# Kernel tuning notes

Hardware: AMD Instinct MI355X
Metric: run time of the kernel (lower is better)

The kernel has to match this reference:

```python
import jax, jax.numpy as jnp
import numpy as np

B, C_IN, C_OUT, H, W = 4, 256, 256, 56, 56
NH, K, P = 2, 5, 2
HD = C_OUT // NH          # 128
SE_H = C_OUT // 16        # 16
SE_H2 = max(SE_H // 16, 1)  # 1
EPS = 1e-5


def setup_inputs() -> dict:
    key = jax.random.key(0)
    ks = jax.random.split(key, 16)
    n = lambda k, sh, s=1.0: jax.random.normal(k, sh, jnp.float32) * s

    def bn_params(k, c):
        k1, k2 = jax.random.split(k)
        return (1.0 + 0.1 * n(k1, (c,)), 0.1 * n(k2, (c,)),
                jnp.zeros((c,), jnp.float32), jnp.ones((c,), jnp.float32))

    agg_g1, agg_b1, agg_m1, agg_v1 = bn_params(ks[6], C_OUT)
    agg_g2, agg_b2, agg_m2, agg_v2 = bn_params(ks[7], C_OUT)
    se_g_in, se_b_in, se_m_in, se_v_in = bn_params(ks[8], SE_H)
    se_g_out, se_b_out, se_m_out, se_v_out = bn_params(ks[9], C_OUT)
    return {
        "x": n(ks[0], (B, C_IN, H, W)),
        "Wq": n(ks[1], (C_OUT, C_IN), C_IN ** -0.5),
        "Wk": n(ks[2], (C_OUT, C_IN), C_IN ** -0.5),
        "Wv": n(ks[3], (C_OUT, C_IN), C_IN ** -0.5),
        "rel_h": n(ks[4], (HD, 1, 1, K, 1)),
        "rel_w": n(ks[5], (HD, 1, 1, 1, K)),
        "agg_g1": agg_g1, "agg_b1": agg_b1, "agg_m1": agg_m1, "agg_v1": agg_v1,
        "agg_W": n(ks[10], (C_OUT, C_OUT), C_OUT ** -0.5),
        "agg_g2": agg_g2, "agg_b2": agg_b2, "agg_m2": agg_m2, "agg_v2": agg_v2,
        "se_Win": n(ks[11], (SE_H, C_OUT), C_OUT ** -0.5),
        "se_g_in": se_g_in, "se_b_in": se_b_in, "se_m_in": se_m_in, "se_v_in": se_v_in,
        "se_fc1": n(ks[12], (SE_H2, SE_H), SE_H ** -0.5),
        "se_fc2": n(ks[13], (SE_H, SE_H2)),
        "se_Wout": n(ks[14], (C_OUT, SE_H), SE_H ** -0.5),
        "se_g_out": se_g_out, "se_b_out": se_b_out, "se_m_out": se_m_out, "se_v_out": se_v_out,
    }


def _conv1x1(Wm, t):
    return jnp.einsum('oc,bchw->bohw', Wm, t)


def _bn(t, g, b, m, v):
    # eval-mode BatchNorm2d with running stats
    return (t - m[:, None, None]) * (g * jax.lax.rsqrt(v + EPS))[:, None, None] + b[:, None, None]


def _windows(t):
    # (B, O, H+2P, W+2P) -> (B, O, H, W, K, K), matching torch unfold(2,K,1).unfold(3,K,1)
    w = jnp.stack([t[:, :, i:i + H, j:j + W] for i in range(K) for j in range(K)], axis=-1)
    return w.reshape(t.shape[0], t.shape[1], H, W, K, K)


def reference(x, Wq, Wk, Wv, rel_h, rel_w,
              agg_g1, agg_b1, agg_m1, agg_v1, agg_W, agg_g2, agg_b2, agg_m2, agg_v2,
              se_Win, se_g_in, se_b_in, se_m_in, se_v_in, se_fc1, se_fc2, se_Wout,
              se_g_out, se_b_out, se_m_out, se_v_out):
    xp = jnp.pad(x, ((0, 0), (0, 0), (P, P), (P, P)))
    q = _conv1x1(Wq, x).reshape(B, NH, HD, H, W)          # (B,NH,HD,H,W)
    k_win = _windows(_conv1x1(Wk, xp))                    # (B,O,H,W,K,K)
    v_win = _windows(_conv1x1(Wv, xp))
    # relative position bias: first head gets rel_h (height taps), second gets rel_w
    k_win = jnp.concatenate([k_win[:, :HD] + rel_h[None], k_win[:, HD:] + rel_w[None]], axis=1)
    k_r = k_win.reshape(B, NH, HD, H, W, K * K)
    v_r = v_win.reshape(B, NH, HD, H, W, K * K)
    scores = jnp.einsum('bnchw,bnchwk->bnhwk', q, k_r) / jnp.sqrt(jnp.float32(HD))
    attn = jax.nn.softmax(scores, axis=-1)
    out = jnp.einsum('bnhwk,bnchwk->bnchw', attn, v_r).reshape(B, C_OUT, H, W)
    # agg: BN -> ReLU -> 1x1 conv -> BN
    y = jax.nn.relu(_bn(out, agg_g1, agg_b1, agg_m1, agg_v1))
    y = _bn(_conv1x1(agg_W, y), agg_g2, agg_b2, agg_m2, agg_v2)
    # squeeze-excitation (intended math; original view(b,c) is a channel-count bug)
    s = jax.nn.relu(_bn(_conv1x1(se_Win, y), se_g_in, se_b_in, se_m_in, se_v_in))  # (B,SE_H,H,W)
    p = s.mean(axis=(2, 3))                                                        # (B,SE_H)
    g = jax.nn.sigmoid(jax.nn.relu(p @ se_fc1.T) @ se_fc2.T)                       # (B,SE_H)
    s = s * g[:, :, None, None]
    return _bn(_conv1x1(se_Wout, s), se_g_out, se_b_out, se_m_out, se_v_out)
```

## Files before the change

### kernel.cpp

```cpp
#include <hip/hip_runtime.h>
#include <hip/hip_bf16.h>

#define HW 3136
#define HH 56
#define WW 56
#define BB 4
#define CC 256
#define HD 128

#define TH 4
#define TW 8
#define WR 8
#define WC 12
#define WPX 96
#define KSTR2 136
#define RSTR 132

#define ASTR 72

typedef __attribute__((ext_vector_type(8))) short bf16x8;
typedef __attribute__((ext_vector_type(4))) float f32x4;

__device__ __forceinline__ unsigned short f2bf(float f) {
    unsigned int u; __builtin_memcpy(&u, &f, 4);
    unsigned int r = u + 0x7FFFu + ((u >> 16) & 1u);
    return (unsigned short)(r >> 16);
}
__device__ __forceinline__ float bflo(unsigned int u) {
    unsigned int x = u << 16; float f; __builtin_memcpy(&f, &x, 4); return f;
}
__device__ __forceinline__ float bfhi(unsigned int u) {
    unsigned int x = u & 0xFFFF0000u; float f; __builtin_memcpy(&f, &x, 4); return f;
}

__global__ __launch_bounds__(256) void xt_cvt(const float* __restrict__ x,
                                              unsigned short* __restrict__ xt)
{
    int b = blockIdx.z;
    int c0 = blockIdx.y * 64;
    int p0 = blockIdx.x * 64;
    __shared__ float tile[64][65];
    int t = threadIdx.x;
    int p4 = t & 15, cl = t >> 4;
    const float* xb = x + ((size_t)b * CC + c0) * HW + p0;
#pragma unroll
    for (int i = 0; i < 4; i++) {
        int c = cl + 16 * i;
        float4 f = *(const float4*)(xb + (size_t)c * HW + p4 * 4);
        tile[c][p4 * 4 + 0] = f.x; tile[c][p4 * 4 + 1] = f.y;
        tile[c][p4 * 4 + 2] = f.z; tile[c][p4 * 4 + 3] = f.w;
    }
    __syncthreads();
    int c2 = t & 31, pl = t >> 5;
    unsigned short* xo = xt + ((size_t)b * HW + p0) * CC + c0;
#pragma unroll
    for (int i = 0; i < 8; i++) {
        int p = pl + 8 * i;
        float a = tile[2 * c2][p], bb = tile[2 * c2 + 1][p];
        unsigned int pk = (unsigned int)f2bf(a) | ((unsigned int)f2bf(bb) << 16);
        *(unsigned int*)(xo + (size_t)p * CC + 2 * c2) = pk;
    }
}

__global__ __launch_bounds__(256) void wcvt(const float* __restrict__ Wq,
                                            const float* __restrict__ Wk,
                                            const float* __restrict__ Wv,
                                            const float* __restrict__ Wa,
                                            const float* __restrict__ Wse,
                                            unsigned short* __restrict__ wb,
                                            float* __restrict__ psum)
{
    int t = threadIdx.x;
    if (blockIdx.y == 4) {
        if (blockIdx.x == 0 && t < 64) psum[t] = 0.f;
        int idx = blockIdx.x * 256 + t;
        if (idx < 1024) {
            float4 f = *(const float4*)(Wse + (size_t)idx * 4);
            uint2 pk;
            pk.x = (unsigned int)f2bf(f.x) | ((unsigned int)f2bf(f.y) << 16);
            pk.y = (unsigned int)f2bf(f.z) | ((unsigned int)f2bf(f.w) << 16);
            *(uint2*)(wb + (size_t)4 * 65536 + (size_t)idx * 4) = pk;
        }
        return;
    }
    const float* srcs[4] = {Wq, Wk, Wv, Wa};
    const float* s = srcs[blockIdx.y];
    int idx = blockIdx.x * 256 + t;
    float4 f = *(const float4*)(s + (size_t)idx * 4);
    uint2 pk;
    pk.x = (unsigned int)f2bf(f.x) | ((unsigned int)f2bf(f.y) << 16);
    pk.y = (unsigned int)f2bf(f.z) | ((unsigned int)f2bf(f.w) << 16);
    *(uint2*)(wb + (size_t)blockIdx.y * 65536 + (size_t)idx * 4) = pk;
}

__global__ __launch_bounds__(256) void qkv_mfma(
    const unsigned short* __restrict__ xt, const unsigned short* __restrict__ wqkv,
    unsigned short* __restrict__ q_ws, unsigned short* __restrict__ k_ws,
    unsigned short* __restrict__ v_ws)
{
    int wsel = blockIdx.z;
    unsigned short* outp = (wsel == 0) ? q_ws : ((wsel == 1) ? k_ws : v_ws);
    int gp0 = blockIdx.x * 128, o0 = blockIdx.y * 128;

    __shared__ unsigned short As[128 * ASTR];
    __shared__ unsigned short Bs[128 * ASTR];
    const unsigned short* xb = xt + (size_t)gp0 * CC;
    const unsigned short* wbp = wqkv + (size_t)wsel * 65536 + (size_t)o0 * CC;

    int t = threadIdx.x;
    int wave = t >> 6, lane = t & 63;
    int mo = (wave & 1) * 64, no = (wave >> 1) * 64;
    int lm = lane & 15, lq = lane >> 4;
    int sr = t >> 3, sc = t & 7;

    f32x4 acc[4][4];
#pragma unroll
    for (int i = 0; i < 4; i++)
#pragma unroll
        for (int j = 0; j < 4; j++) acc[i][j] = (f32x4){0.f, 0.f, 0.f, 0.f};

    for (int k0 = 0; k0 < 256; k0 += 64) {
#pragma unroll
        for (int i = 0; i < 4; i++) {
            int r = sr + 32 * i;
            *(uint4*)&As[r * ASTR + sc * 8] = *(const uint4*)(xb + (size_t)r * CC + k0 + sc * 8);
            *(uint4*)&Bs[r * ASTR + sc * 8] = *(const uint4*)(wbp + (size_t)r * CC + k0 + sc * 8);
        }
        __syncthreads();
#pragma unroll
        for (int ks = 0; ks < 64; ks += 32) {
            bf16x8 af[4], bfr[4];
#pragma unroll
            for (int i = 0; i < 4; i++)
                af[i] = *(bf16x8*)&As[(mo + 16 * i + lm) * ASTR + ks + lq * 8];
#pragma unroll
            for (int j = 0; j < 4; j++)
                bfr[j] = *(bf16x8*)&Bs[(no + 16 * j + lm) * ASTR + ks + lq * 8];
#pragma unroll
            for (int i = 0; i < 4; i++)
#pragma unroll
                for (int j = 0; j < 4; j++)
                    acc[i][j] = __builtin_amdgcn_mfma_f32_16x16x32_bf16(
                        af[i], bfr[j], acc[i][j], 0, 0, 0);
        }
        __syncthreads();
    }
    unsigned short* ob = outp + (size_t)gp0 * CC + o0;
    bool ev = (lm & 1) == 0;
    int elm = lm & ~1;
#pragma unroll
    for (int i = 0; i < 4; i++)
#pragma unroll
        for (int j = 0; j < 4; j++)
#pragma unroll
            for (int r = 0; r < 4; r++) {
                float v = acc[i][j][r];
                float p = __shfl_xor(v, 1, 64);
                unsigned int pk = ev
                    ? ((unsigned int)f2bf(v) | ((unsigned int)f2bf(p) << 16))
                    : ((unsigned int)f2bf(p) | ((unsigned int)f2bf(v) << 16));
                if (ev == (r < 2)) {
                    int m = mo + 16 * i + lq * 4 + r;
                    int n = no + 16 * j + elm;
                    *(unsigned int*)(ob + (size_t)m * CC + n) = pk;
                }
            }
}

__global__ __launch_bounds__(256) void agg_mfma(
    const unsigned short* __restrict__ ao, const unsigned short* __restrict__ wagg,
    const float* __restrict__ g1, const float* __restrict__ b1,
    const float* __restrict__ m1, const float* __restrict__ v1,
    const float* __restrict__ g2, const float* __restrict__ b2,
    const float* __restrict__ m2, const float* __restrict__ v2,
    float* __restrict__ y2)
{
    int gp0 = blockIdx.x * 128, o0 = blockIdx.y * 128;

    __shared__ unsigned short As[128 * ASTR];
    __shared__ unsigned short Bs[128 * ASTR];
    __shared__ float s1[256], o1[256], s2[256], o2[256];

    int t = threadIdx.x;
    {
        float sc1 = g1[t] * rsqrtf(v1[t] + 1e-5f);
        s1[t] = sc1; o1[t] = b1[t] - m1[t] * sc1;
        float sc2 = g2[t] * rsqrtf(v2[t] + 1e-5f);
        s2[t] = sc2; o2[t] = b2[t] - m2[t] * sc2;
    }

    const unsigned short* aob = ao + (size_t)gp0 * CC;
    const unsigned short* wbp = wagg + (size_t)o0 * CC;

    int wave = t >> 6, lane = t & 63;
    int mo = (wave & 1) * 64, no = (wave >> 1) * 64;
    int lm = lane & 15, lq = lane >> 4;
    int sr = t >> 3, sc = t & 7;

    f32x4 acc[4][4];
#pragma unroll
    for (int i = 0; i < 4; i++)
#pragma unroll
        for (int j = 0; j < 4; j++) acc[i][j] = (f32x4){0.f, 0.f, 0.f, 0.f};

    __syncthreads();

    for (int k0 = 0; k0 < 256; k0 += 64) {
#pragma unroll
        for (int i = 0; i < 4; i++) {
            int r = sr + 32 * i;
            int cb = k0 + sc * 8;
            uint4 u = *(const uint4*)(aob + (size_t)r * CC + cb);
            float e[8] = {bflo(u.x), bfhi(u.x), bflo(u.y), bfhi(u.y),
                          bflo(u.z), bfhi(u.z), bflo(u.w), bfhi(u.w)};
            unsigned short pk[8];
#pragma unroll
            for (int uu = 0; uu < 8; uu++) {
                float vv = fmaxf(e[uu] * s1[cb + uu] + o1[cb + uu], 0.f);
                pk[uu] = f2bf(vv);
            }
            *(uint4*)&As[r * ASTR + sc * 8] = *(uint4*)pk;
            *(uint4*)&Bs[r * ASTR + sc * 8] = *(const uint4*)(wbp + (size_t)r * CC + k0 + sc * 8);
        }
        __syncthreads();
#pragma unroll
        for (int ks = 0; ks < 64; ks += 32) {
            bf16x8 af[4], bfr[4];
#pragma unroll
            for (int i = 0; i < 4; i++)
                af[i] = *(bf16x8*)&As[(mo + 16 * i + lm) * ASTR + ks + lq * 8];
#pragma unroll
            for (int j = 0; j < 4; j++)
                bfr[j] = *(bf16x8*)&Bs[(no + 16 * j + lm) * ASTR + ks + lq * 8];
#pragma unroll
            for (int i = 0; i < 4; i++)
#pragma unroll
                for (int j = 0; j < 4; j++)
                    acc[i][j] = __builtin_amdgcn_mfma_f32_16x16x32_bf16(
                        af[i], bfr[j], acc[i][j], 0, 0, 0);
        }
        __syncthreads();
    }
    float* yb = y2 + (size_t)gp0 * CC + o0;
#pragma unroll
    for (int i = 0; i < 4; i++)
#pragma unroll
        for (int j = 0; j < 4; j++)
#pragma unroll
            for (int r = 0; r < 4; r++) {
                int m = mo + 16 * i + lq * 4 + r;
                int n = no + 16 * j + lm;
                yb[(size_t)m * CC + n] = acc[i][j][r] * s2[o0 + n] + o2[o0 + n];
            }
}

__global__ __launch_bounds__(256) void attn_kernel(
    const unsigned short* __restrict__ q_ws, const unsigned short* __restrict__ k_ws,
    const unsigned short* __restrict__ v_ws,
    const float* __restrict__ rel_h, const float* __restrict__ rel_w,
    unsigned short* __restrict__ ao_ws)
{
    __shared__ unsigned short kwin[WPX * KSTR2];
    __shared__ float relT[5 * RSTR];

    int t = threadIdx.x;
    int tile = blockIdx.x;
    int n = blockIdx.y;
    int b = blockIdx.z;
    int tr = tile / 7, tc = tile - tr * 7;
    int h0 = tr * TH, w0 = tc * TW;
    const float* rel = (n == 0) ? rel_h : rel_w;
    const size_t base = (size_t)b * HW * CC + n * HD;

    {
        int c8 = t & 15, pw0 = t >> 4;
#pragma unroll
        for (int it = 0; it < 6; it++) {
            int pw = pw0 + it * 16;
            int wr = pw / 12, wc = pw - wr * 12;
            int gh = h0 + wr - 2, gw = w0 + wc - 2;
            uint4 u = make_uint4(0u, 0u, 0u, 0u);
            if (gh >= 0 && gh < HH && gw >= 0 && gw < WW)
                u = *(const uint4*)(k_ws + base + (size_t)(gh * WW + gw) * CC + c8 * 8);
            *(uint4*)&kwin[pw * KSTR2 + c8 * 8] = u;
        }
        if (t < 128) {
#pragma unroll
            for (int tt = 0; tt < 5; tt++)
                relT[tt * RSTR + t] = rel[t * 5 + tt];
        }
    }
    __syncthreads();

    int px = t >> 3, c4g = t & 7;
    int pr = px >> 3, pc = px & 7;
    int ghp = h0 + pr, gwp = w0 + pc;
    const size_t pbase = base + (size_t)(ghp * WW + gwp) * CC;

    float4 q4[4];
#pragma unroll
    for (int i = 0; i < 4; i++) {
        uint2 uq = *(const uint2*)(q_ws + pbase + (c4g + 8 * i) * 4);
        q4[i] = make_float4(bflo(uq.x), bfhi(uq.x), bflo(uq.y), bfhi(uq.y));
    }

    float acc[30];
#pragma unroll
    for (int tt = 0; tt < 30; tt++) acc[tt] = 0.f;
#pragma unroll
    for (int i = 0; i < 4; i++) {
        float4 q = q4[i];
        int co = (c4g + 8 * i) * 4;
#pragma unroll
        for (int tt = 0; tt < 25; tt++) {
            int di = tt / 5, dj = tt - 5 * (tt / 5);
            int wpx = (pr + di) * WC + pc + dj;
            uint2 ku = *(const uint2*)&kwin[wpx * KSTR2 + co];
            acc[tt] += q.x * bflo(ku.x) + q.y * bfhi(ku.x)
                     + q.z * bflo(ku.y) + q.w * bfhi(ku.y);
        }
#pragma unroll
        for (int tt = 0; tt < 5; tt++) {
            float4 r4 = *(const float4*)&relT[tt * RSTR + co];
            acc[25 + tt] += q.x * r4.x + q.y * r4.y + q.z * r4.z + q.w * r4.w;
        }
    }
#pragma unroll
    for (int tt = 0; tt < 30; tt++) {
#pragma unroll
        for (int m = 1; m < 8; m <<= 1)
            acc[tt] += __shfl_xor(acc[tt], m, 64);
    }
    {
        const float inv = 0.08838834764831845f;
        float mx = -1e30f;
#pragma unroll
        for (int tt = 0; tt < 25; tt++) {
            int di = tt / 5, dj = tt - 5 * (tt / 5);
            acc[tt] = (acc[tt] + ((n == 0) ? acc[25 + di] : acc[25 + dj])) * inv;
            mx = fmaxf(mx, acc[tt]);
        }
        float sum = 0.f;
#pragma unroll
        for (int tt = 0; tt < 25; tt++) { acc[tt] = __expf(acc[tt] - mx); sum += acc[tt]; }
        float rs = 1.f / sum;
#pragma unroll
        for (int tt = 0; tt < 25; tt++) acc[tt] *= rs;
    }
    __syncthreads();

    {
        int c8 = t & 15, pw0 = t >> 4;
#pragma unroll
        for (int it = 0; it < 6; it++) {
            int pw = pw0 + it * 16;
            int wr = pw / 12, wc = pw - wr * 12;
            int gh = h0 + wr - 2, gw = w0 + wc - 2;
            uint4 u = make_uint4(0u, 0u, 0u, 0u);
            if (gh >= 0 && gh < HH && gw >= 0 && gw < WW)
                u = *(const uint4*)(v_ws + base + (size_t)(gh * WW + gw) * CC + c8 * 8);
            *(uint4*)&kwin[pw * KSTR2 + c8 * 8] = u;
        }
    }
    __syncthreads();

    float4 oacc[4];
#pragma unroll
    for (int i = 0; i < 4; i++) oacc[i] = make_float4(0.f, 0.f, 0.f, 0.f);
#pragma unroll
    for (int tt = 0; tt < 25; tt++) {
        int di = tt / 5, dj = tt - 5 * (tt / 5);
        int wpx = (pr + di) * WC + pc + dj;
        float a = acc[tt];
#pragma unroll
        for (int i = 0; i < 4; i++) {
            uint2 vu = *(const uint2*)&kwin[wpx * KSTR2 + (c4g + 8 * i) * 4];
            oacc[i].x += a * bflo(vu.x); oacc[i].y += a * bfhi(vu.x);
            oacc[i].z += a * bflo(vu.y); oacc[i].w += a * bfhi(vu.y);
        }
    }
#pragma unroll
    for (int i = 0; i < 4; i++) {
        uint2 pk;
        pk.x = (unsigned int)f2bf(oacc[i].x) | ((unsigned int)f2bf(oacc[i].y) << 16);
        pk.y = (unsigned int)f2bf(oacc[i].z) | ((unsigned int)f2bf(oacc[i].w) << 16);
        *(uint2*)(ao_ws + pbase + (c4g + 8 * i) * 4) = pk;
    }
}

__global__ __launch_bounds__(256) void se_in_mfma(
    const float* __restrict__ y2, const unsigned short* __restrict__ wse,
    const float* __restrict__ gin, const float* __restrict__ bin,
    const float* __restrict__ min_, const float* __restrict__ vin,
    float* __restrict__ s_ws, float* __restrict__ psum)
{
    int wave = threadIdx.x >> 6, lane = threadIdx.x & 63;
    int tile = blockIdx.x * 4 + wave;
    int gp0 = tile * 16;
    int b = tile / 196;
    int lm = lane & 15, lq = lane >> 4;

    f32x4 acc = (f32x4){0.f, 0.f, 0.f, 0.f};
    const float* ya = y2 + (size_t)(gp0 + lm) * CC;
#pragma unroll
    for (int k0 = 0; k0 < 256; k0 += 32) {
        int kb = k0 + lq * 8;
        float4 f0 = *(const float4*)(ya + kb);
        float4 f1 = *(const float4*)(ya + kb + 4);
        unsigned short pk[8] = {f2bf(f0.x), f2bf(f0.y), f2bf(f0.z), f2bf(f0.w),
                                f2bf(f1.x), f2bf(f1.y), f2bf(f1.z), f2bf(f1.w)};
        bf16x8 af = *(bf16x8*)pk;
        bf16x8 bf = *(const bf16x8*)(wse + (size_t)lm * CC + kb);
        acc = __builtin_amdgcn_mfma_f32_16x16x32_bf16(af, bf, acc, 0, 0, 0);
    }
    float sc = gin[lm] * rsqrtf(vin[lm] + 1e-5f);
    float off = bin[lm] - min_[lm] * sc;
    float sum4 = 0.f;
#pragma unroll
    for (int r = 0; r < 4; r++) {
        int row = lq * 4 + r;
        float v = fmaxf(acc[r] * sc + off, 0.f);
        s_ws[(size_t)(gp0 + row) * 16 + lm] = v;
        sum4 += v;
    }
    sum4 += __shfl_xor(sum4, 16, 64);
    sum4 += __shfl_xor(sum4, 32, 64);
    if (lane < 16) atomicAdd(&psum[b * 16 + lane], sum4);
}

__global__ __launch_bounds__(256) void se_out_kernel(
    const float* __restrict__ s_ws, const float* __restrict__ psum,
    const float* __restrict__ fc1, const float* __restrict__ fc2,
    const float* __restrict__ se_Wout,
    const float* __restrict__ gout, const float* __restrict__ bout,
    const float* __restrict__ mout, const float* __restrict__ vout,
    float* __restrict__ out)
{
    int b = blockIdx.y;
    int px0 = blockIdx.x * 32;
    __shared__ float sl[32 * 17];
    __shared__ float wg[256 * 20];
    __shared__ float bo[256];
    __shared__ float gg[16];
    int t = threadIdx.x;

    if (t < 16) {
        float h = 0.f;
#pragma unroll
        for (int jj = 0; jj < 16; jj++)
            h += (psum[b * 16 + jj] * (1.f / 3136.f)) * fc1[jj];
        h = fmaxf(h, 0.f);
        float z = h * fc2[t];
        gg[t] = 1.f / (1.f + __expf(-z));
    }
    {
        const float* sb = s_ws + (size_t)(b * HW + px0) * 16;
#pragma unroll
        for (int i = 0; i < 2; i++) {
            int idx = t + 256 * i;
            sl[(idx >> 4) * 17 + (idx & 15)] = sb[idx];
        }
    }
    __syncthreads();
    {
        float sc = gout[t] * rsqrtf(vout[t] + 1e-5f);
        bo[t] = bout[t] - mout[t] * sc;
        const float* wr = se_Wout + (size_t)t * 16;
#pragma unroll
        for (int k = 0; k < 16; k++)
            wg[t * 20 + k] = wr[k] * gg[k] * sc;
    }
    __syncthreads();

    int px = t & 31, og = t >> 5;
    float4 s0 = *(float4*)&sl[px * 17 + 0];
    float4 s1v = *(float4*)&sl[px * 17 + 4];
    float4 s2v = *(float4*)&sl[px * 17 + 8];
    float4 s3 = *(float4*)&sl[px * 17 + 12];
    float* ob = out + (size_t)b * CC * HW + px0 + px;
#pragma unroll
    for (int oi = 0; oi < 32; oi++) {
        int o = og * 32 + oi;
        float4 w0 = *(float4*)&wg[o * 20 + 0];
        float4 w1 = *(float4*)&wg[o * 20 + 4];
        float4 w2 = *(float4*)&wg[o * 20 + 8];
        float4 w3 = *(float4*)&wg[o * 20 + 12];
        float r = bo[o]
            + s0.x * w0.x + s0.y * w0.y + s0.z * w0.z + s0.w * w0.w
            + s1v.x * w1.x + s1v.y * w1.y + s1v.z * w1.z + s1v.w * w1.w
            + s2v.x * w2.x + s2v.y * w2.y + s2v.z * w2.z + s2v.w * w2.w
            + s3.x * w3.x + s3.y * w3.y + s3.z * w3.z + s3.w * w3.w;
        ob[(size_t)o * HW] = r;
    }
}

extern "C" void kernel_launch(void* const* d_in, const int* in_sizes, int n_in,
                              void* d_out, int out_size, void* d_ws, size_t ws_size,
                              hipStream_t stream) {
    const float* x     = (const float*)d_in[0];
    const float* Wq    = (const float*)d_in[1];
    const float* Wk    = (const float*)d_in[2];
    const float* Wv    = (const float*)d_in[3];
    const float* rel_h = (const float*)d_in[4];
    const float* rel_w = (const float*)d_in[5];
    const float* agg_g1 = (const float*)d_in[6];
    const float* agg_b1 = (const float*)d_in[7];
    const float* agg_m1 = (const float*)d_in[8];
    const float* agg_v1 = (const float*)d_in[9];
    const float* agg_W  = (const float*)d_in[10];
    const float* agg_g2 = (const float*)d_in[11];
    const float* agg_b2 = (const float*)d_in[12];
    const float* agg_m2 = (const float*)d_in[13];
    const float* agg_v2 = (const float*)d_in[14];
    const float* se_Win = (const float*)d_in[15];
    const float* se_g_in = (const float*)d_in[16];
    const float* se_b_in = (const float*)d_in[17];
    const float* se_m_in = (const float*)d_in[18];
    const float* se_v_in = (const float*)d_in[19];
    const float* se_fc1  = (const float*)d_in[20];
    const float* se_fc2  = (const float*)d_in[21];
    const float* se_Wout = (const float*)d_in[22];
    const float* se_g_out = (const float*)d_in[23];
    const float* se_b_out = (const float*)d_in[24];
    const float* se_m_out = (const float*)d_in[25];
    const float* se_v_out = (const float*)d_in[26];

    const size_t NQ = (size_t)BB * HW * CC;
    unsigned short* q_ws  = (unsigned short*)d_ws;
    unsigned short* k_ws  = q_ws + NQ;
    unsigned short* v_ws  = k_ws + NQ;
    unsigned short* ao_ws = v_ws + NQ;
    unsigned short* xt    = ao_ws;
    float* y2_ws = (float*)d_ws;
    float* s_ws  = (float*)(ao_ws + NQ);
    float* psum  = s_ws + (size_t)BB * HW * 16;
    unsigned short* wbf = (unsigned short*)(psum + 64);

    xt_cvt<<<dim3(49, 4, 4), 256, 0, stream>>>(x, xt);
    wcvt<<<dim3(64, 5), 256, 0, stream>>>(Wq, Wk, Wv, agg_W, se_Win, wbf, psum);
    qkv_mfma<<<dim3(98, 2, 3), 256, 0, stream>>>(xt, wbf, q_ws, k_ws, v_ws);
    attn_kernel<<<dim3(98, 2, 4), 256, 0, stream>>>(q_ws, k_ws, v_ws, rel_h, rel_w, ao_ws);
    agg_mfma<<<dim3(98, 2), 256, 0, stream>>>(ao_ws, wbf + 3 * 65536,
        agg_g1, agg_b1, agg_m1, agg_v1, agg_g2, agg_b2, agg_m2, agg_v2, y2_ws);
    se_in_mfma<<<dim3(196), 256, 0, stream>>>(y2_ws, wbf + 4 * 65536,
        se_g_in, se_b_in, se_m_in, se_v_in, s_ws, psum);
    se_out_kernel<<<dim3(98, 4), 256, 0, stream>>>(s_ws, psum, se_fc1, se_fc2,
        se_Wout, se_g_out, se_b_out, se_m_out, se_v_out, (float*)d_out);
}
```

Baseline: 211.1 us.

## Halve attention tile height and give each thread 8 contiguous channels

The attention kernel tile shrinks from 4x8 to 2x8 pixels, and the grid doubles to 196 tiles per image. Each pixel now gets 16 threads, each owning 8 contiguous channels, instead of 8 threads with four strided 4-channel slices. This allows 128-bit LDS and global loads and more blocks for latency hiding. The cost is extra halo loading per output pixel (a 6x12 window for 16 pixels) and one more shuffle-reduction stage per score.

Measured after the change: 199.6 us. 1.06x faster.

```diff
diff --git a/kernel.cpp b/kernel.cpp
--- a/kernel.cpp
+++ b/kernel.cpp
@@ -8,11 +8,11 @@
 #define CC 256
 #define HD 128
 
-#define TH 4
+#define TH 2
 #define TW 8
-#define WR 8
+#define WR 6
 #define WC 12
-#define WPX 96
+#define WPX 72
 #define KSTR2 136
 #define RSTR 132
 
@@ -273,16 +273,18 @@
     const size_t base = (size_t)b * HW * CC + n * HD;
 
     {
-        int c8 = t & 15, pw0 = t >> 4;
-#pragma unroll
-        for (int it = 0; it < 6; it++) {
-            int pw = pw0 + it * 16;
-            int wr = pw / 12, wc = pw - wr * 12;
-            int gh = h0 + wr - 2, gw = w0 + wc - 2;
-            uint4 u = make_uint4(0u, 0u, 0u, 0u);
-            if (gh >= 0 && gh < HH && gw >= 0 && gw < WW)
-                u = *(const uint4*)(k_ws + base + (size_t)(gh * WW + gw) * CC + c8 * 8);
-            *(uint4*)&kwin[pw * KSTR2 + c8 * 8] = u;
+        int c16 = t & 15, pwt = t >> 4;
+#pragma unroll
+        for (int it = 0; it < 5; it++) {
+            int pw = pwt + it * 16;
+            if (pw < WPX) {
+                int wr = pw / 12, wc = pw - wr * 12;
+                int gh = h0 + wr - 2, gw = w0 + wc - 2;
+                uint4 u = make_uint4(0u, 0u, 0u, 0u);
+                if (gh >= 0 && gh < HH && gw >= 0 && gw < WW)
+                    u = *(const uint4*)(k_ws + base + (size_t)(gh * WW + gw) * CC + c16 * 8);
+                *(uint4*)&kwin[pw * KSTR2 + c16 * 8] = u;
+            }
         }
         if (t < 128) {
 #pragma unroll
@@ -292,43 +294,40 @@
     }
     __syncthreads();
 
-    int px = t >> 3, c4g = t & 7;
+    int px = t >> 4, cg = t & 15;
     int pr = px >> 3, pc = px & 7;
     int ghp = h0 + pr, gwp = w0 + pc;
     const size_t pbase = base + (size_t)(ghp * WW + gwp) * CC;
 
-    float4 q4[4];
-#pragma unroll
-    for (int i = 0; i < 4; i++) {
-        uint2 uq = *(const uint2*)(q_ws + pbase + (c4g + 8 * i) * 4);
-        q4[i] = make_float4(bflo(uq.x), bfhi(uq.x), bflo(uq.y), bfhi(uq.y));
+    float q[8];
+    {
+        uint4 uq = *(const uint4*)(q_ws + pbase + cg * 8);
+        q[0] = bflo(uq.x); q[1] = bfhi(uq.x); q[2] = bflo(uq.y); q[3] = bfhi(uq.y);
+        q[4] = bflo(uq.z); q[5] = bfhi(uq.z); q[6] = bflo(uq.w); q[7] = bfhi(uq.w);
     }
 
     float acc[30];
 #pragma unroll
-    for (int tt = 0; tt < 30; tt++) acc[tt] = 0.f;
-#pragma unroll
-    for (int i = 0; i < 4; i++) {
-        float4 q = q4[i];
-        int co = (c4g + 8 * i) * 4;
-#pragma unroll
-        for (int tt = 0; tt < 25; tt++) {
-            int di = tt / 5, dj = tt - 5 * (tt / 5);
-            int wpx = (pr + di) * WC + pc + dj;
-            uint2 ku = *(const uint2*)&kwin[wpx * KSTR2 + co];
-            acc[tt] += q.x * bflo(ku.x) + q.y * bfhi(ku.x)
-                     + q.z * bflo(ku.y) + q.w * bfhi(ku.y);
-        }
-#pragma unroll
-        for (int tt = 0; tt < 5; tt++) {
-            float4 r4 = *(const float4*)&relT[tt * RSTR + co];
-            acc[25 + tt] += q.x * r4.x + q.y * r4.y + q.z * r4.z + q.w * r4.w;
-        }
+    for (int tt = 0; tt < 25; tt++) {
+        int di = tt / 5, dj = tt - 5 * (tt / 5);
+        int wpx = (pr + di) * WC + pc + dj;
+        uint4 ku = *(const uint4*)&kwin[wpx * KSTR2 + cg * 8];
+        acc[tt] = q[0] * bflo(ku.x) + q[1] * bfhi(ku.x)
+                + q[2] * bflo(ku.y) + q[3] * bfhi(ku.y)
+                + q[4] * bflo(ku.z) + q[5] * bfhi(ku.z)
+                + q[6] * bflo(ku.w) + q[7] * bfhi(ku.w);
+    }
+#pragma unroll
+    for (int tt = 0; tt < 5; tt++) {
+        float4 r0 = *(const float4*)&relT[tt * RSTR + cg * 8];
+        float4 r1 = *(const float4*)&relT[tt * RSTR + cg * 8 + 4];
+        acc[25 + tt] = q[0] * r0.x + q[1] * r0.y + q[2] * r0.z + q[3] * r0.w
+                     + q[4] * r1.x + q[5] * r1.y + q[6] * r1.z + q[7] * r1.w;
     }
 #pragma unroll
     for (int tt = 0; tt < 30; tt++) {
 #pragma unroll
-        for (int m = 1; m < 8; m <<= 1)
+        for (int m = 1; m < 16; m <<= 1)
             acc[tt] += __shfl_xor(acc[tt], m, 64);
     }
     {
@@ -350,42 +349,42 @@
     __syncthreads();
 
     {
-        int c8 = t & 15, pw0 = t >> 4;
-#pragma unroll
-        for (int it = 0; it < 6; it++) {
-            int pw = pw0 + it * 16;
-            int wr = pw / 12, wc = pw - wr * 12;
-            int gh = h0 + wr - 2, gw = w0 + wc - 2;
-            uint4 u = make_uint4(0u, 0u, 0u, 0u);
-            if (gh >= 0 && gh < HH && gw >= 0 && gw < WW)
-                u = *(const uint4*)(v_ws + base + (size_t)(gh * WW + gw) * CC + c8 * 8);
-            *(uint4*)&kwin[pw * KSTR2 + c8 * 8] = u;
-        }
-    }
-    __syncthreads();
-
-    float4 oacc[4];
-#pragma unroll
-    for (int i = 0; i < 4; i++) oacc[i] = make_float4(0.f, 0.f, 0.f, 0.f);
+        int c16 = t & 15, pwt = t >> 4;
+#pragma unroll
+        for (int it = 0; it < 5; it++) {
+            int pw = pwt + it * 16;
+            if (pw < WPX) {
+                int wr = pw / 12, wc = pw - wr * 12;
+                int gh = h0 + wr - 2, gw = w0 + wc - 2;
+                uint4 u = make_uint4(0u, 0u, 0u, 0u);
+                if (gh >= 0 && gh < HH && gw >= 0 && gw < WW)
+                    u = *(const uint4*)(v_ws + base + (size_t)(gh * WW + gw) * CC + c16 * 8);
+                *(uint4*)&kwin[pw * KSTR2 + c16 * 8] = u;
+            }
+        }
+    }
+    __syncthreads();
+
+    float o[8];
+#pragma unroll
+    for (int i = 0; i < 8; i++) o[i] = 0.f;
 #pragma unroll
     for (int tt = 0; tt < 25; tt++) {
         int di = tt / 5, dj = tt - 5 * (tt / 5);
         int wpx = (pr + di) * WC + pc + dj;
         float a = acc[tt];
-#pragma unroll
-        for (int i = 0; i < 4; i++) {
-            uint2 vu = *(const uint2*)&kwin[wpx * KSTR2 + (c4g + 8 * i) * 4];
-            oacc[i].x += a * bflo(vu.x); oacc[i].y += a * bfhi(vu.x);
-            oacc[i].z += a * bflo(vu.y); oacc[i].w += a * bfhi(vu.y);
-        }
-    }
-#pragma unroll
-    for (int i = 0; i < 4; i++) {
-        uint2 pk;
-        pk.x = (unsigned int)f2bf(oacc[i].x) | ((unsigned int)f2bf(oacc[i].y) << 16);
-        pk.y = (unsigned int)f2bf(oacc[i].z) | ((unsigned int)f2bf(oacc[i].w) << 16);
-        *(uint2*)(ao_ws + pbase + (c4g + 8 * i) * 4) = pk;
-    }
+        uint4 vu = *(const uint4*)&kwin[wpx * KSTR2 + cg * 8];
+        o[0] += a * bflo(vu.x); o[1] += a * bfhi(vu.x);
+        o[2] += a * bflo(vu.y); o[3] += a * bfhi(vu.y);
+        o[4] += a * bflo(vu.z); o[5] += a * bfhi(vu.z);
+        o[6] += a * bflo(vu.w); o[7] += a * bfhi(vu.w);
+    }
+    uint4 pk;
+    pk.x = (unsigned int)f2bf(o[0]) | ((unsigned int)f2bf(o[1]) << 16);
+    pk.y = (unsigned int)f2bf(o[2]) | ((unsigned int)f2bf(o[3]) << 16);
+    pk.z = (unsigned int)f2bf(o[4]) | ((unsigned int)f2bf(o[5]) << 16);
+    pk.w = (unsigned int)f2bf(o[6]) | ((unsigned int)f2bf(o[7]) << 16);
+    *(uint4*)(ao_ws + pbase + cg * 8) = pk;
 }
 
 __global__ __launch_bounds__(256) void se_in_mfma(
@@ -539,7 +538,7 @@
     xt_cvt<<<dim3(49, 4, 4), 256, 0, stream>>>(x, xt);
     wcvt<<<dim3(64, 5), 256, 0, stream>>>(Wq, Wk, Wv, agg_W, se_Win, wbf, psum);
     qkv_mfma<<<dim3(98, 2, 3), 256, 0, stream>>>(xt, wbf, q_ws, k_ws, v_ws);
-    attn_kernel<<<dim3(98, 2, 4), 256, 0, stream>>>(q_ws, k_ws, v_ws, rel_h, rel_w, ao_ws);
+    attn_kernel<<<dim3(196, 2, 4), 256, 0, stream>>>(q_ws, k_ws, v_ws, rel_h, rel_w, ao_ws);
     agg_mfma<<<dim3(98, 2), 256, 0, stream>>>(ao_ws, wbf + 3 * 65536,
         agg_g1, agg_b1, agg_m1, agg_v1, agg_g2, agg_b2, agg_m2, agg_v2, y2_ws);
     se_in_mfma<<<dim3(196), 256, 0, stream>>>(y2_ws, wbf + 4 * 65536,
```
